# Performance work log

Hardware: AMD Instinct MI355X
Metric: run time of the kernel (lower is better)

Reference implementation:

```python
import jax, jax.numpy as jnp
import numpy as np

B, H, W, NC = 8, 64, 64, 128
INTER = NC // 2
BN_EPS = 1e-4


def setup_inputs() -> dict:
    key = jax.random.key(0)
    ks = jax.random.split(key, 6)
    s_in = 1.0 / np.sqrt(NC)
    s_w = 1.0 / np.sqrt(INTER)
    return {
        "x": jax.random.normal(ks[0], (B, H, W, NC), jnp.float32),
        "theta_w": jax.random.normal(ks[1], (NC, INTER), jnp.float32) * s_in,
        "theta_b": jnp.zeros((INTER,), jnp.float32),
        "phi_w": jax.random.normal(ks[2], (NC, INTER), jnp.float32) * s_in,
        "phi_b": jnp.zeros((INTER,), jnp.float32),
        "g_w": jax.random.normal(ks[3], (NC, INTER), jnp.float32) * s_in,
        "g_b": jnp.zeros((INTER,), jnp.float32),
        "W_w": jax.random.normal(ks[4], (INTER, NC), jnp.float32) * s_w,
        "W_b": jnp.zeros((NC,), jnp.float32),
        "bn_gamma": jnp.ones((NC,), jnp.float32),
        "bn_beta": jnp.zeros((NC,), jnp.float32),
        "bn_mean": jnp.zeros((NC,), jnp.float32),
        "bn_var": jax.random.uniform(ks[5], (NC,), jnp.float32, 0.5, 1.5),
    }


def reference(x, theta_w, theta_b, phi_w, phi_b, g_w, g_b, W_w, W_b,
              bn_gamma, bn_beta, bn_mean, bn_var):
    b, h, w, c = x.shape
    n = h * w
    # 1x1 conv projections == per-pixel GEMMs; flatten spatial to tokens
    xt = x.reshape(b, n, c)                                  # [B, N, C]
    theta = xt @ theta_w + theta_b                           # [B, N, C']
    phi = xt @ phi_w + phi_b                                 # [B, N, C']
    g = xt @ g_w + g_b                                       # [B, N, C']
    # single-head, unscaled non-local attention
    f = jnp.einsum("bnc,bmc->bnm", theta, phi)               # [B, N, N]
    attn = jax.nn.softmax(f, axis=-1)
    y = jnp.einsum("bnm,bmc->bnc", attn, g)                  # [B, N, C']
    # W: 1x1 conv back to nc + BatchNorm (inference), then residual
    wy = y @ W_w + W_b                                       # [B, N, C]
    inv = bn_gamma * jax.lax.rsqrt(bn_var + BN_EPS)
    wy = (wy - bn_mean) * inv + bn_beta
    z = wy.reshape(b, h, w, c) + x
    return z
```

## Files before the change

kernel.cpp:

```cpp
#include <hip/hip_runtime.h>
#include <math.h>

typedef _Float16 v8h __attribute__((ext_vector_type(8)));
typedef __fp16 h2 __attribute__((ext_vector_type(2)));
typedef float v4f __attribute__((ext_vector_type(4)));
typedef float v16f __attribute__((ext_vector_type(16)));

#define MFMA32(a, b, c) __builtin_amdgcn_mfma_f32_32x32x16_f16((a), (b), (c), 0, 0, 0)
#define MFMA16(a, b, c) __builtin_amdgcn_mfma_f32_16x16x32_f16((a), (b), (c), 0, 0, 0)
#define ZV4 ((v4f){0.f, 0.f, 0.f, 0.f})
#define LOG2E 1.44269504f

#define TA64(row, colb)  ((((row) * 128) + (colb)) ^ (((row) & 7) << 4))
#define TA128(row, colb) ((((row) * 256) + (colb)) ^ (((row) & 15) << 4))

#define RAW_BARRIER() do {                                        \
    asm volatile("s_waitcnt lgkmcnt(0)" ::: "memory");            \
    asm volatile("s_barrier" ::: "memory");                       \
} while (0)

__device__ __forceinline__ unsigned int pk_f16(float a, float b) {
    return __builtin_bit_cast(unsigned int, __builtin_amdgcn_cvt_pkrtz(a, b));
}
__device__ __forceinline__ void pl32swap(unsigned int& a, unsigned int& b) {
    asm("v_permlane32_swap_b32 %0, %1" : "+v"(a), "+v"(b));
}
__device__ __forceinline__ float fexp2(float x) {
    float r;
    asm("v_exp_f32 %0, %1" : "=v"(r) : "v"(x));
    return r;
}

__global__ __launch_bounds__(256) void k_prep(
    const float* __restrict__ tw, const float* __restrict__ pw,
    const float* __restrict__ gw,
    const float* __restrict__ Ww, const float* __restrict__ Wb,
    const float* __restrict__ gamma, const float* __restrict__ beta,
    const float* __restrict__ mean, const float* __restrict__ var,
    _Float16* __restrict__ Wt, _Float16* __restrict__ wallT,
    float* __restrict__ sc, float* __restrict__ bi)
{
    int gid = blockIdx.x * 256 + threadIdx.x;
    #pragma unroll
    for (int r = 0; r < 2; ++r) {
        int idx = r * 4096 + gid;
        int d = idx >> 7, c = idx & 127;
        Wt[c * 64 + d] = (_Float16)Ww[idx];
    }
    #pragma unroll
    for (int r = 0; r < 6; ++r) {
        int idx = r * 4096 + gid;
        int p = idx >> 13, rem = idx & 8191;
        int o = rem >> 7, k = rem & 127;
        const float* wm = (p == 0) ? tw : (p == 1) ? pw : gw;
        wallT[idx] = (_Float16)wm[k * 64 + o];
    }
    if (blockIdx.x == 0 && threadIdx.x < 128) {
        int c = threadIdx.x;
        float inv = gamma[c] * rsqrtf(var[c] + 1e-4f);
        sc[c] = inv;
        bi[c] = (Wb[c] - mean[c]) * inv + beta[c];
    }
}

__global__ __launch_bounds__(512, 4) void k_proj(
    const float* __restrict__ x, const _Float16* __restrict__ wallT,
    const float* __restrict__ tb, const float* __restrict__ pb,
    const float* __restrict__ gb,
    _Float16* __restrict__ theta, _Float16* __restrict__ phi,
    _Float16* __restrict__ gT)
{
    __shared__ __align__(16) _Float16 tsc[8][16 * 72];
    __shared__ __align__(16) _Float16 gblk[64][136];
    const int t = threadIdx.x;
    const int w = t >> 6, l = t & 63, h = l >> 4, lo = l & 15;
    const int tok0 = blockIdx.x * 128 + w * 16;
    _Float16* tw_l = &tsc[w][0];

    v8h xA[4];
    #pragma unroll
    for (int kc = 0; kc < 4; ++kc) {
        const float* px = x + (size_t)(tok0 + lo) * 128 + kc * 32 + h * 8;
        float4 f0 = *(const float4*)(px);
        float4 f1 = *(const float4*)(px + 4);
        uint4 u;
        u.x = pk_f16(f0.x, f0.y); u.y = pk_f16(f0.z, f0.w);
        u.z = pk_f16(f1.x, f1.y); u.w = pk_f16(f1.z, f1.w);
        xA[kc] = __builtin_bit_cast(v8h, u);
    }

    #pragma unroll
    for (int p = 0; p < 2; ++p) {
        const _Float16* wp = wallT + p * 8192;
        const float* bias = (p == 0) ? tb : pb;
        _Float16* dst = (p == 0) ? theta : phi;
        const float scale = (p == 0) ? LOG2E : 1.0f;
        #pragma unroll
        for (int oc = 0; oc < 4; ++oc) {
            int o = oc * 16 + lo;
            v4f acc = ZV4;
            #pragma unroll
            for (int kc = 0; kc < 4; ++kc) {
                v8h B = *(const v8h*)(wp + o * 128 + kc * 32 + h * 8);
                acc = MFMA16(xA[kc], B, acc);
            }
            float bv = bias[o];
            #pragma unroll
            for (int rr = 0; rr < 4; ++rr)
                tw_l[(4 * h + rr) * 72 + o] = (_Float16)((acc[rr] + bv) * scale);
        }
        int token = l >> 2, c = l & 3;
        v8h v0 = *(const v8h*)&tw_l[token * 72 + c * 16];
        v8h v1 = *(const v8h*)&tw_l[token * 72 + c * 16 + 8];
        _Float16* dp = dst + (size_t)(tok0 + token) * 64 + c * 16;
        *(v8h*)(dp) = v0;
        *(v8h*)(dp + 8) = v1;
    }
    {
        const _Float16* wp = wallT + 2 * 8192;
        #pragma unroll
        for (int oc = 0; oc < 4; ++oc) {
            v4f acc = ZV4;
            #pragma unroll
            for (int kc = 0; kc < 4; ++kc) {
                v8h A = *(const v8h*)(wp + (oc * 16 + lo) * 128 + kc * 32 + h * 8);
                acc = MFMA16(A, xA[kc], acc);
            }
            #pragma unroll
            for (int rr = 0; rr < 4; ++rr) {
                int o = oc * 16 + 4 * h + rr;
                gblk[o][w * 16 + lo] = (_Float16)(acc[rr] + gb[o]);
            }
        }
    }
    __syncthreads();
    {
        int o = t >> 3, ch = t & 7;
        v8h v0 = *(const v8h*)&gblk[o][ch * 16];
        v8h v1 = *(const v8h*)&gblk[o][ch * 16 + 8];
        int tokg0 = blockIdx.x * 128;
        int bb = tokg0 >> 12, n0 = (tokg0 & 4095) + ch * 16;
        _Float16* gp = gT + ((size_t)bb * 64 + o) * 4096 + n0;
        *(v8h*)(gp) = v0;
        *(v8h*)(gp + 8) = v1;
    }
}

__global__ __launch_bounds__(512, 2) void k_attn(
    const _Float16* __restrict__ theta,
    const _Float16* __restrict__ phi,
    const _Float16* __restrict__ gT,
    const _Float16* __restrict__ Wt,
    const float* __restrict__ sc, const float* __restrict__ bi,
    const float* __restrict__ x, float* __restrict__ out)
{
    __shared__ __align__(16) _Float16 ldsbuf[32768];
    __shared__ float zf[8 * 64];

    const int t = threadIdx.x;
    const int w = t >> 6, l = t & 63, q32 = l & 31, hi2 = l >> 5;
    const int qp = w & 1, kh = w >> 1;
    const int bid = blockIdx.x;
    const int b = bid & 7, qb = bid >> 3;
    const size_t tok0 = (size_t)b * 4096 + qb * 128;

    char* phB = (char*)ldsbuf;
    char* gvB = (char*)ldsbuf + 32768;

    v8h thB[2][4];
    #pragma unroll
    for (int f = 0; f < 2; ++f)
        #pragma unroll
        for (int kc = 0; kc < 4; ++kc)
            thB[f][kc] = *(const v8h*)(theta +
                (tok0 + qp * 64 + f * 32 + q32) * 64 + kc * 16 + hi2 * 8);

    const _Float16* phb = phi + (size_t)b * 4096 * 64;
    const _Float16* gvb = gT + (size_t)b * 64 * 4096;

    v16f yacc[2][2];
    #pragma unroll
    for (int f = 0; f < 2; ++f)
        #pragma unroll
        for (int df = 0; df < 2; ++df)
            #pragma unroll
            for (int r = 0; r < 16; ++r) yacc[f][df][r] = 0.f;
    float mrow[2] = {-INFINITY, -INFINITY}, lpart[2] = {0.f, 0.f};

    int qkRd[4], gvRd[2][2];
    #pragma unroll
    for (int kc = 0; kc < 4; ++kc)
        qkRd[kc] = TA64(kh * 32 + q32, (kc * 16 + hi2 * 8) * 2);
    #pragma unroll
    for (int df = 0; df < 2; ++df)
        #pragma unroll
        for (int s = 0; s < 2; ++s)
            gvRd[df][s] = TA128(df * 32 + q32, (kh * 32 + s * 16 + hi2 * 8) * 2);

    const int phA0 = TA64(t >> 3, (t & 7) * 16);
    const int phA1 = TA64((t >> 3) + 64, (t & 7) * 16);
    const int gvA0 = TA128(t >> 4, (t & 15) * 16);
    const int gvA1 = TA128((t >> 4) + 32, (t & 15) * 16);
    const _Float16* pPh = phb + (size_t)(t >> 3) * 64 + (t & 7) * 8;
    const _Float16* pGv = gvb + (size_t)(t >> 4) * 4096 + (t & 15) * 8;

    v8h pf0 = *(const v8h*)(pPh);
    v8h pf1 = *(const v8h*)(pPh + 64 * 64);
    v8h pf2 = *(const v8h*)(pGv);
    v8h pf3 = *(const v8h*)(pGv + (size_t)32 * 4096);
    pPh += 8192; pGv += 128;

    for (int kt = 0; kt < 32; ++kt) {
        char* phL = phB + (kt & 1) * 16384;
        char* gvL = gvB + (kt & 1) * 16384;
        *(v8h*)(phL + phA0) = pf0;
        *(v8h*)(phL + phA1) = pf1;
        *(v8h*)(gvL + gvA0) = pf2;
        *(v8h*)(gvL + gvA1) = pf3;
        if (kt < 31) {
            pf0 = *(const v8h*)(pPh);
            pf1 = *(const v8h*)(pPh + 64 * 64);
            pf2 = *(const v8h*)(pGv);
            pf3 = *(const v8h*)(pGv + (size_t)32 * 4096);
            pPh += 8192; pGv += 128;
        }
        RAW_BARRIER();
        v16f S0, S1;
        #pragma unroll
        for (int r = 0; r < 16; ++r) { S0[r] = 0.f; S1[r] = 0.f; }
        __builtin_amdgcn_s_setprio(1);
        #pragma unroll
        for (int kc = 0; kc < 4; ++kc) {
            v8h A = *(const v8h*)(phL + qkRd[kc]);
            S0 = MFMA32(A, thB[0][kc], S0);
            S1 = MFMA32(A, thB[1][kc], S1);
        }
        __builtin_amdgcn_s_setprio(0);
        float vmax[2];
        {
            float a0 = fmaxf(fmaxf(S0[0], S0[1]), S0[2]);
            float a1 = fmaxf(fmaxf(S0[3], S0[4]), S0[5]);
            float a2 = fmaxf(fmaxf(S0[6], S0[7]), S0[8]);
            float a3 = fmaxf(fmaxf(S0[9], S0[10]), S0[11]);
            float a4 = fmaxf(fmaxf(S0[12], S0[13]), S0[14]);
            float v = fmaxf(fmaxf(fmaxf(a0, a1), fmaxf(a2, a3)),
                            fmaxf(a4, S0[15]));
            vmax[0] = fmaxf(v, __shfl_xor(v, 32));
        }
        {
            float a0 = fmaxf(fmaxf(S1[0], S1[1]), S1[2]);
            float a1 = fmaxf(fmaxf(S1[3], S1[4]), S1[5]);
            float a2 = fmaxf(fmaxf(S1[6], S1[7]), S1[8]);
            float a3 = fmaxf(fmaxf(S1[9], S1[10]), S1[11]);
            float a4 = fmaxf(fmaxf(S1[12], S1[13]), S1[14]);
            float v = fmaxf(fmaxf(fmaxf(a0, a1), fmaxf(a2, a3)),
                            fmaxf(a4, S1[15]));
            vmax[1] = fmaxf(v, __shfl_xor(v, 32));
        }
        bool ok = (vmax[0] <= mrow[0] + 11.54f) && (vmax[1] <= mrow[1] + 11.54f);
        if (!__all(ok)) {
            #pragma unroll
            for (int f = 0; f < 2; ++f) {
                float mn = fmaxf(mrow[f], vmax[f]);
                float aa = fexp2(mrow[f] - mn);
                mrow[f] = mn;
                lpart[f] *= aa;
                #pragma unroll
                for (int df = 0; df < 2; ++df)
                    #pragma unroll
                    for (int r = 0; r < 16; ++r)
                        yacc[f][df][r] *= aa;
            }
        }
        v8h pB[2][2];
        #pragma unroll
        for (int f = 0; f < 2; ++f) {
            v16f& S = (f == 0) ? S0 : S1;
            float psum = 0.f;
            #pragma unroll
            for (int r = 0; r < 16; ++r) {
                S[r] = fexp2(S[r] - mrow[f]);
                psum += S[r];
            }
            lpart[f] += psum;
            unsigned int W0 = pk_f16(S[0], S[1]),   W1 = pk_f16(S[2], S[3]);
            unsigned int W2 = pk_f16(S[4], S[5]),   W3 = pk_f16(S[6], S[7]);
            unsigned int W4 = pk_f16(S[8], S[9]),   W5 = pk_f16(S[10], S[11]);
            unsigned int W6 = pk_f16(S[12], S[13]), W7 = pk_f16(S[14], S[15]);
            pl32swap(W0, W2); pl32swap(W1, W3);
            pl32swap(W4, W6); pl32swap(W5, W7);
            uint4 u1; u1.x = W0; u1.y = W1; u1.z = W2; u1.w = W3;
            uint4 u2; u2.x = W4; u2.y = W5; u2.z = W6; u2.w = W7;
            pB[f][0] = __builtin_bit_cast(v8h, u1);
            pB[f][1] = __builtin_bit_cast(v8h, u2);
        }
        __builtin_amdgcn_s_setprio(1);
        #pragma unroll
        for (int df = 0; df < 2; ++df)
            #pragma unroll
            for (int s = 0; s < 2; ++s) {
                v8h A = *(const v8h*)(gvL + gvRd[df][s]);
                yacc[0][df] = MFMA32(A, pB[0][s], yacc[0][df]);
                yacc[1][df] = MFMA32(A, pB[1][s], yacc[1][df]);
            }
        __builtin_amdgcn_s_setprio(0);
    }

    __syncthreads();
    #pragma unroll
    for (int f = 0; f < 2; ++f) {
        float lrow = lpart[f] + __shfl_xor(lpart[f], 32);
        float inv = 1.0f / lrow;
        char* slot = (char*)ldsbuf + w * 8192 + f * 4096 + l * 64;
        #pragma unroll
        for (int j = 0; j < 4; ++j) {
            int df = j >> 1, r0 = (j & 1) * 8;
            uint4 u;
            u.x = pk_f16(yacc[f][df][r0 + 0] * inv, yacc[f][df][r0 + 1] * inv);
            u.y = pk_f16(yacc[f][df][r0 + 2] * inv, yacc[f][df][r0 + 3] * inv);
            u.z = pk_f16(yacc[f][df][r0 + 4] * inv, yacc[f][df][r0 + 5] * inv);
            u.w = pk_f16(yacc[f][df][r0 + 6] * inv, yacc[f][df][r0 + 7] * inv);
            *(uint4*)(slot + (j * 16 ^ ((l & 3) << 4))) = u;
        }
        zf[(w * 2 + f) * 32 + q32] = mrow[f] + __log2f(lrow);
    }
    __syncthreads();
    if (w >= 2) return;

    #pragma unroll
    for (int f = 0; f < 2; ++f) {
        float zq[4];
        #pragma unroll
        for (int kp = 0; kp < 4; ++kp)
            zq[kp] = zf[((kp * 2 + w) * 2 + f) * 32 + q32];
        float zmx = fmaxf(fmaxf(zq[0], zq[1]), fmaxf(zq[2], zq[3]));
        float wsum = 0.f;
        float yfin[2][16];
        #pragma unroll
        for (int df = 0; df < 2; ++df)
            #pragma unroll
            for (int r = 0; r < 16; ++r) yfin[df][r] = 0.f;
        #pragma unroll
        for (int kp = 0; kp < 4; ++kp) {
            char* slot = (char*)ldsbuf + (kp * 2 + w) * 8192 + f * 4096 + l * 64;
            float wk = fexp2(zq[kp] - zmx);
            wsum += wk;
            #pragma unroll
            for (int j = 0; j < 4; ++j) {
                v8h c = *(const v8h*)(slot + (j * 16 ^ ((l & 3) << 4)));
                int df = j >> 1, r0 = (j & 1) * 8;
                #pragma unroll
                for (int e = 0; e < 8; ++e)
                    yfin[df][r0 + e] += wk * (float)c[e];
            }
        }
        float nrm = 1.0f / wsum;
        v8h yA[4];
        #pragma unroll
        for (int kc = 0; kc < 4; ++kc) {
            int df = kc >> 1, r0 = (kc & 1) * 8;
            unsigned int Wa = pk_f16(yfin[df][r0 + 0] * nrm, yfin[df][r0 + 1] * nrm);
            unsigned int Wb2 = pk_f16(yfin[df][r0 + 2] * nrm, yfin[df][r0 + 3] * nrm);
            unsigned int Wc = pk_f16(yfin[df][r0 + 4] * nrm, yfin[df][r0 + 5] * nrm);
            unsigned int Wd = pk_f16(yfin[df][r0 + 6] * nrm, yfin[df][r0 + 7] * nrm);
            pl32swap(Wa, Wc); pl32swap(Wb2, Wd);
            uint4 u; u.x = Wa; u.y = Wb2; u.z = Wc; u.w = Wd;
            yA[kc] = __builtin_bit_cast(v8h, u);
        }
        const int tokA = qb * 128 + w * 64 + f * 32;
        const float* xb = x + (size_t)b * 4096 * 128;
        float* ob = out + (size_t)b * 4096 * 128;
        #pragma unroll
        for (int cf = 0; cf < 4; ++cf) {
            int c = cf * 32 + q32;
            v16f wy;
            #pragma unroll
            for (int r = 0; r < 16; ++r) wy[r] = 0.f;
            #pragma unroll
            for (int kc = 0; kc < 4; ++kc) {
                v8h wB = *(const v8h*)(Wt + c * 64 + kc * 16 + hi2 * 8);
                wy = MFMA32(yA[kc], wB, wy);
            }
            float scc = sc[c], bic = bi[c];
            #pragma unroll
            for (int r = 0; r < 16; ++r) {
                int qrow = (r & 3) + 8 * (r >> 2) + 4 * hi2;
                size_t off = (size_t)(tokA + qrow) * 128 + c;
                ob[off] = wy[r] * scc + bic + xb[off];
            }
        }
    }
}

extern "C" void kernel_launch(void* const* d_in, const int* in_sizes, int n_in,
                              void* d_out, int out_size, void* d_ws, size_t ws_size,
                              hipStream_t stream) {
    const float* x     = (const float*)d_in[0];
    const float* tw    = (const float*)d_in[1];
    const float* tb    = (const float*)d_in[2];
    const float* pw    = (const float*)d_in[3];
    const float* pb    = (const float*)d_in[4];
    const float* gw    = (const float*)d_in[5];
    const float* gb    = (const float*)d_in[6];
    const float* Ww    = (const float*)d_in[7];
    const float* Wb    = (const float*)d_in[8];
    const float* gamma = (const float*)d_in[9];
    const float* beta  = (const float*)d_in[10];
    const float* mean  = (const float*)d_in[11];
    const float* var   = (const float*)d_in[12];

    char* ws = (char*)d_ws;
    _Float16* theta = (_Float16*)ws;
    _Float16* phi   = (_Float16*)(ws + (4u << 20));
    _Float16* gT    = (_Float16*)(ws + (8u << 20));
    _Float16* Wt    = (_Float16*)(ws + (12u << 20));
    _Float16* wallT = (_Float16*)(ws + (12u << 20) + (1u << 16));
    float* sc       = (float*)(ws + (12u << 20) + (2u << 16));
    float* bi       = sc + 128;

    k_prep<<<16, 256, 0, stream>>>(tw, pw, gw, Ww, Wb, gamma, beta, mean, var,
                                   Wt, wallT, sc, bi);
    k_proj<<<256, 512, 0, stream>>>(x, wallT, tb, pb, gb, theta, phi, gT);
    k_attn<<<256, 512, 0, stream>>>(theta, phi, gT, Wt, sc, bi,
                                    x, (float*)d_out);
}
```

Baseline: 82.72 us.

## Hoist G LDS loads and interleave per-fragment softmax with PV MFMAs

Loads the G operand fragments from LDS right after the QK MFMAs, so their latency overlaps the max reduction. The exp/pack/PV-MFMA work is split per fragment, letting the first fragment's MFMAs run while the second fragment's exponentials are computed. The row sum is now taken with fdot2 over the packed fp16 probabilities instead of fp32 adds, which removes some VALU adds. The cost is higher register pressure from holding the gA fragments, and the row sum now uses the fp16-rounded values.

Measured after the change: 82.28 us, median of 3. About the same (-0.5%).

```diff
diff --git a/kernel.cpp b/kernel.cpp
--- a/kernel.cpp
+++ b/kernel.cpp
@@ -236,6 +236,12 @@
             S1 = MFMA32(A, thB[1][kc], S1);
         }
         __builtin_amdgcn_s_setprio(0);
+        v8h gA[2][2];
+        #pragma unroll
+        for (int df = 0; df < 2; ++df)
+            #pragma unroll
+            for (int s = 0; s < 2; ++s)
+                gA[df][s] = *(const v8h*)(gvL + gvRd[df][s]);
         float vmax[2];
         {
             float a0 = fmaxf(fmaxf(S0[0], S0[1]), S0[2]);
@@ -272,38 +278,71 @@
                         yacc[f][df][r] *= aa;
             }
         }
-        v8h pB[2][2];
-        #pragma unroll
-        for (int f = 0; f < 2; ++f) {
-            v16f& S = (f == 0) ? S0 : S1;
+        const h2 one2 = {(__fp16)1.0f, (__fp16)1.0f};
+        {
+            #pragma unroll
+            for (int r = 0; r < 16; ++r) S0[r] = fexp2(S0[r] - mrow[0]);
             float psum = 0.f;
-            #pragma unroll
-            for (int r = 0; r < 16; ++r) {
-                S[r] = fexp2(S[r] - mrow[f]);
-                psum += S[r];
-            }
-            lpart[f] += psum;
-            unsigned int W0 = pk_f16(S[0], S[1]),   W1 = pk_f16(S[2], S[3]);
-            unsigned int W2 = pk_f16(S[4], S[5]),   W3 = pk_f16(S[6], S[7]);
-            unsigned int W4 = pk_f16(S[8], S[9]),   W5 = pk_f16(S[10], S[11]);
-            unsigned int W6 = pk_f16(S[12], S[13]), W7 = pk_f16(S[14], S[15]);
+            h2 pk[8];
+            #pragma unroll
+            for (int j = 0; j < 8; ++j) {
+                pk[j] = __builtin_amdgcn_cvt_pkrtz(S0[2 * j], S0[2 * j + 1]);
+                psum = __builtin_amdgcn_fdot2(pk[j], one2, psum, false);
+            }
+            lpart[0] += psum;
+            unsigned int W0 = __builtin_bit_cast(unsigned int, pk[0]);
+            unsigned int W1 = __builtin_bit_cast(unsigned int, pk[1]);
+            unsigned int W2 = __builtin_bit_cast(unsigned int, pk[2]);
+            unsigned int W3 = __builtin_bit_cast(unsigned int, pk[3]);
+            unsigned int W4 = __builtin_bit_cast(unsigned int, pk[4]);
+            unsigned int W5 = __builtin_bit_cast(unsigned int, pk[5]);
+            unsigned int W6 = __builtin_bit_cast(unsigned int, pk[6]);
+            unsigned int W7 = __builtin_bit_cast(unsigned int, pk[7]);
             pl32swap(W0, W2); pl32swap(W1, W3);
             pl32swap(W4, W6); pl32swap(W5, W7);
             uint4 u1; u1.x = W0; u1.y = W1; u1.z = W2; u1.w = W3;
             uint4 u2; u2.x = W4; u2.y = W5; u2.z = W6; u2.w = W7;
-            pB[f][0] = __builtin_bit_cast(v8h, u1);
-            pB[f][1] = __builtin_bit_cast(v8h, u2);
-        }
-        __builtin_amdgcn_s_setprio(1);
-        #pragma unroll
-        for (int df = 0; df < 2; ++df)
-            #pragma unroll
-            for (int s = 0; s < 2; ++s) {
-                v8h A = *(const v8h*)(gvL + gvRd[df][s]);
-                yacc[0][df] = MFMA32(A, pB[0][s], yacc[0][df]);
-                yacc[1][df] = MFMA32(A, pB[1][s], yacc[1][df]);
-            }
-        __builtin_amdgcn_s_setprio(0);
+            v8h pB0 = __builtin_bit_cast(v8h, u1);
+            v8h pB1 = __builtin_bit_cast(v8h, u2);
+            __builtin_amdgcn_s_setprio(1);
+            yacc[0][0] = MFMA32(gA[0][0], pB0, yacc[0][0]);
+            yacc[0][0] = MFMA32(gA[0][1], pB1, yacc[0][0]);
+            yacc[0][1] = MFMA32(gA[1][0], pB0, yacc[0][1]);
+            yacc[0][1] = MFMA32(gA[1][1], pB1, yacc[0][1]);
+            __builtin_amdgcn_s_setprio(0);
+        }
+        {
+            #pragma unroll
+            for (int r = 0; r < 16; ++r) S1[r] = fexp2(S1[r] - mrow[1]);
+            float psum = 0.f;
+            h2 pk[8];
+            #pragma unroll
+            for (int j = 0; j < 8; ++j) {
+                pk[j] = __builtin_amdgcn_cvt_pkrtz(S1[2 * j], S1[2 * j + 1]);
+                psum = __builtin_amdgcn_fdot2(pk[j], one2, psum, false);
+            }
+            lpart[1] += psum;
+            unsigned int W0 = __builtin_bit_cast(unsigned int, pk[0]);
+            unsigned int W1 = __builtin_bit_cast(unsigned int, pk[1]);
+            unsigned int W2 = __builtin_bit_cast(unsigned int, pk[2]);
+            unsigned int W3 = __builtin_bit_cast(unsigned int, pk[3]);
+            unsigned int W4 = __builtin_bit_cast(unsigned int, pk[4]);
+            unsigned int W5 = __builtin_bit_cast(unsigned int, pk[5]);
+            unsigned int W6 = __builtin_bit_cast(unsigned int, pk[6]);
+            unsigned int W7 = __builtin_bit_cast(unsigned int, pk[7]);
+            pl32swap(W0, W2); pl32swap(W1, W3);
+            pl32swap(W4, W6); pl32swap(W5, W7);
+            uint4 u1; u1.x = W0; u1.y = W1; u1.z = W2; u1.w = W3;
+            uint4 u2; u2.x = W4; u2.y = W5; u2.z = W6; u2.w = W7;
+            v8h pB0 = __builtin_bit_cast(v8h, u1);
+            v8h pB1 = __builtin_bit_cast(v8h, u2);
+            __builtin_amdgcn_s_setprio(1);
+            yacc[1][0] = MFMA32(gA[0][0], pB0, yacc[1][0]);
+            yacc[1][0] = MFMA32(gA[0][1], pB1, yacc[1][0]);
+            yacc[1][1] = MFMA32(gA[1][0], pB0, yacc[1][1]);
+            yacc[1][1] = MFMA32(gA[1][1], pB1, yacc[1][1]);
+            __builtin_amdgcn_s_setprio(0);
+        }
     }
 
     __syncthreads();
```
